# Kernel optimization log

Measured on AMD Instinct MI355X. Metric: run time of the kernel, lower is better.

Reference implementation:

```python
import jax, jax.numpy as jnp
import numpy as np

WS = 7        # window_size
SHIFT = 3     # shift_size
NH = 12       # num_heads
DIM = 384
HID = 1536    # int(dim * 4.0)
EPS = 1e-5


def _rel_index(ws):
    # relative_position_index exactly as in the torch __init__ (static, numpy)
    c = np.stack(np.meshgrid(np.arange(ws), np.arange(ws), indexing='ij')).reshape(2, -1)
    r = c[:, :, None] - c[:, None, :]            # (2, N, N)
    return jnp.asarray((r[0] + ws - 1) * (2 * ws - 1) + (r[1] + ws - 1))  # (N, N) int


def _swin_attn_mask(H, W, ws, sh):
    # standard Swin shifted-window mask: 0 within region, -100 across regions
    img = np.zeros((H, W))
    cnt = 0
    for hs in (slice(0, H - ws), slice(H - ws, H - sh), slice(H - sh, H)):
        for wsl in (slice(0, W - ws), slice(W - ws, W - sh), slice(W - sh, W)):
            img[hs, wsl] = cnt
            cnt += 1
    mw = img.reshape(H // ws, ws, W // ws, ws).transpose(0, 2, 1, 3).reshape(-1, ws * ws)
    am = mw[:, None, :] - mw[:, :, None]
    return jnp.asarray(np.where(am != 0, -100.0, 0.0).astype(np.float32))  # (nW, N, N)


def _ln(x, g, b):
    m = x.mean(-1, keepdims=True)
    v = ((x - m) ** 2).mean(-1, keepdims=True)
    return (x - m) / jnp.sqrt(v + EPS) * g + b


def setup_inputs() -> dict:
    key = jax.random.key(0)
    ks = jax.random.split(key, 12)
    B, H, W, C = 32, 56, 56, DIM
    x = jax.random.normal(ks[0], (B, H * W, C), dtype=jnp.float32)
    return {
        'x': x,
        'attn_mask': _swin_attn_mask(H, W, WS, SHIFT),
        'norm1_g': jnp.ones((C,), jnp.float32),
        'norm1_b': jnp.zeros((C,), jnp.float32),
        'qkv_w': jax.random.normal(ks[1], (C, 3 * C), jnp.float32) * 0.02,
        'qkv_b': jnp.zeros((3 * C,), jnp.float32),
        'rpb_table': jax.random.normal(ks[2], ((2 * WS - 1) ** 2, NH), jnp.float32) * 0.02,
        'proj_w': jax.random.normal(ks[3], (C, C), jnp.float32) * 0.02,
        'proj_b': jnp.zeros((C,), jnp.float32),
        'norm2_g': jnp.ones((C,), jnp.float32),
        'norm2_b': jnp.zeros((C,), jnp.float32),
        'fc1_w': jax.random.normal(ks[4], (C, HID), jnp.float32) * 0.02,
        'fc1_b': jnp.zeros((HID,), jnp.float32),
        'fc2_w': jax.random.normal(ks[5], (HID, C), jnp.float32) * 0.02,
        'fc2_b': jnp.zeros((C,), jnp.float32),
        'H': 56,
        'W': 56,
    }


def reference(x, attn_mask, norm1_g, norm1_b, qkv_w, qkv_b, rpb_table,
              proj_w, proj_b, norm2_g, norm2_b, fc1_w, fc1_b, fc2_w, fc2_b, H, W):
    B, L, C = x.shape
    hd = C // NH
    scale = hd ** -0.5
    N = WS * WS

    residual = x
    h = _ln(x, norm1_g, norm1_b).reshape(B, H, W, C)
    h = jnp.roll(h, (-SHIFT, -SHIFT), axis=(1, 2))
    # window partition -> (B*nW, N, C)
    win = h.reshape(B, H // WS, WS, W // WS, WS, C).transpose(0, 1, 3, 2, 4, 5)
    win = win.reshape(-1, N, C)
    Bn = win.shape[0]

    qkv = (win @ qkv_w + qkv_b).reshape(Bn, N, 3, NH, hd)
    q, k, v = jnp.moveaxis(qkv, 2, 0)            # each (Bn, N, NH, hd)
    q = q.transpose(0, 2, 1, 3) * scale          # (Bn, NH, N, hd)
    k = k.transpose(0, 2, 1, 3)
    v = v.transpose(0, 2, 1, 3)

    attn = jnp.einsum('bhnd,bhmd->bhnm', q, k)   # (Bn, NH, N, N)
    bias = rpb_table[_rel_index(WS)]             # (N, N, NH)
    attn = attn + bias.transpose(2, 0, 1)[None]

    nW = attn_mask.shape[0]
    attn = attn.reshape(Bn // nW, nW, NH, N, N) + attn_mask[None, :, None]
    attn = jax.nn.softmax(attn.reshape(Bn, NH, N, N), axis=-1)

    out = jnp.einsum('bhnm,bhmd->bhnd', attn, v).transpose(0, 2, 1, 3).reshape(Bn, N, C)
    out = out @ proj_w + proj_b

    # window reverse -> (B, H, W, C)
    out = out.reshape(B, H // WS, W // WS, WS, WS, C).transpose(0, 1, 3, 2, 4, 5)
    out = out.reshape(B, H, W, C)
    out = jnp.roll(out, (SHIFT, SHIFT), axis=(1, 2)).reshape(B, H * W, C)

    x = residual + out
    h2 = _ln(x, norm2_g, norm2_b)
    mlp = jax.nn.gelu(h2 @ fc1_w + fc1_b, approximate=False) @ fc2_w + fc2_b
    return x + mlp
```

## Files before the change

### kernel.cpp

```cpp
#include <hip/hip_runtime.h>
#include <stdint.h>
#include <math.h>

typedef unsigned short u16;
typedef unsigned int u32;
using short8 = __attribute__((ext_vector_type(8))) short;
using f32x4  = __attribute__((ext_vector_type(4))) float;

#define NHEADS 12
#define NTOK 49
#define CDIM 384
#define HIDDIM 1536
#define HDIM 32
#define BNWIN 2048
#define MROWS 100352
#define QKV_STRIDE ((size_t)BNWIN * NHEADS * NTOK * HDIM)
#define ATT_SCALE 0.17677669529663687f
#define AW 4

__device__ __forceinline__ float bf2f(u16 u) {
    union { unsigned int i; float f; } z; z.i = ((unsigned int)u) << 16; return z.f;
}
__device__ __forceinline__ u16 f2bf(float f) {
    union { float f; unsigned int i; } z; z.f = f;
    unsigned int i = z.i;
    i += 0x7FFFu + ((i >> 16) & 1u);
    return (u16)(i >> 16);
}
__device__ __forceinline__ float lo16(u32 u) {
    union { u32 i; float f; } z; z.i = u << 16; return z.f;
}
__device__ __forceinline__ float hi16(u32 u) {
    union { u32 i; float f; } z; z.i = u & 0xffff0000u; return z.f;
}

__device__ __forceinline__ void async16(const void* g, void* l) {
    __builtin_amdgcn_global_load_lds(
        (const __attribute__((address_space(1))) void*)g,
        (__attribute__((address_space(3))) void*)l, 16, 0, 0);
}

__global__ __launch_bounds__(256) void k_conv(const float* __restrict__ B,
    u16* __restrict__ BT, int K, int N)
{
    const int idx = blockIdx.x * 256 + threadIdx.x;
    if (idx >= K * N) return;
    const int n = idx / K, k = idx - n * K;
    BT[idx] = f2bf(B[(size_t)k * N + n]);
}

__global__ __launch_bounds__(256) void k_btab(const float* __restrict__ rpb,
    float* __restrict__ bt)
{
    const int idx = blockIdx.x * 256 + threadIdx.x;
    const int r    = idx & 3;
    const int lane = (idx >> 2) & 63;
    const int tile = (idx >> 8) & 15;
    const int h    = (idx >> 12) % NHEADS;
    const int cls  = idx / (NHEADS << 12);
    const int mt = tile >> 2, nt = tile & 3;
    const int kt = mt * 16 + (lane >> 4) * 4 + r;
    const int qt = nt * 16 + (lane & 15);
    float val;
    if (kt >= NTOK) val = -1e30f;
    else if (qt >= NTOK) val = 0.f;
    else {
        const int pk = kt / 7, qk = kt % 7, pq = qt / 7, qq = qt % 7;
        val = rpb[((pq - pk + 6) * 13 + (qq - qk + 6)) * NHEADS + h];
        const int ae = cls >> 1, be = cls & 1;
        const int regq = (ae ? ((pq < 4) ? 1 : 2) : 0) * 3 + (be ? ((qq < 4) ? 1 : 2) : 0);
        const int regk = (ae ? ((pk < 4) ? 1 : 2) : 0) * 3 + (be ? ((qk < 4) ? 1 : 2) : 0);
        if (regq != regk) val -= 100.f;
    }
    bt[idx] = val;
}

__global__ __launch_bounds__(256) void k_ln1(const float* __restrict__ x,
    const float* __restrict__ g, const float* __restrict__ b, u16* __restrict__ outw)
{
    const int lane = threadIdx.x & 63;
    const int t = blockIdx.x * 4 + (threadIdx.x >> 6);
    const int wi = t / NTOK, n = t % NTOK;
    const int bb = wi >> 6, w64 = wi & 63;
    const int p = (w64 >> 3) * 7 + n / 7;
    const int q = (w64 & 7) * 7 + n % 7;
    const int sh = (p + 3) % 56, sw = (q + 3) % 56;
    const float* row = x + ((size_t)bb * 3136 + sh * 56 + sw) * CDIM;
    float v[6]; float s = 0.f, sq = 0.f;
#pragma unroll
    for (int i = 0; i < 6; i++) {
        v[i] = row[lane + 64 * i];
        s += v[i]; sq += v[i] * v[i];
    }
#pragma unroll
    for (int off = 32; off >= 1; off >>= 1) {
        s  += __shfl_xor(s, off, 64);
        sq += __shfl_xor(sq, off, 64);
    }
    const float mean = s * (1.f / CDIM);
    const float var  = sq * (1.f / CDIM) - mean * mean;
    const float rstd = rsqrtf(var + 1e-5f);
    u16* orow = outw + (size_t)t * CDIM;
#pragma unroll
    for (int i = 0; i < 6; i++) {
        const int c = lane + 64 * i;
        orow[c] = f2bf((v[i] - mean) * rstd * g[c] + b[c]);
    }
}

__global__ __launch_bounds__(256) void k_ln2(const float* __restrict__ y,
    const float* __restrict__ g, const float* __restrict__ b, u16* __restrict__ outw)
{
    const int lane = threadIdx.x & 63;
    const int t = blockIdx.x * 4 + (threadIdx.x >> 6);
    const float* row = y + (size_t)t * CDIM;
    float v[6]; float s = 0.f, sq = 0.f;
#pragma unroll
    for (int i = 0; i < 6; i++) {
        v[i] = row[lane + 64 * i];
        s += v[i]; sq += v[i] * v[i];
    }
#pragma unroll
    for (int off = 32; off >= 1; off >>= 1) {
        s  += __shfl_xor(s, off, 64);
        sq += __shfl_xor(sq, off, 64);
    }
    const float mean = s * (1.f / CDIM);
    const float var  = sq * (1.f / CDIM) - mean * mean;
    const float rstd = rsqrtf(var + 1e-5f);
    u16* orow = outw + (size_t)t * CDIM;
#pragma unroll
    for (int i = 0; i < 6; i++) {
        const int c = lane + 64 * i;
        orow[c] = f2bf((v[i] - mean) * rstd * g[c] + b[c]);
    }
}

template<int MODE>
__global__ __launch_bounds__(256) void k_mgemm(
    const u16* __restrict__ A, const u16* __restrict__ BT,
    const float* __restrict__ bias,
    u16* __restrict__ out_bf,
    const float* res_f,
    float* out_f,
    int M, int Nn, int K)
{
    __shared__ __align__(16) u16 Als[128 * 32];
    __shared__ __align__(16) u16 Bls[128 * 32];
    const int tid = threadIdx.x;
    const int w = tid >> 6, l = tid & 63;
    const int wr = w >> 1, wc = w & 1;
    const int lrow = l & 15, quad = l >> 4;
    const int m0 = blockIdx.x * 128, n0 = blockIdx.y * 128;

    const int seg0 = tid, seg1 = tid + 256;
    const int r0 = seg0 >> 2, q0 = (seg0 & 3) ^ ((r0 >> 1) & 3);
    const int r1 = seg1 >> 2, q1 = (seg1 & 3) ^ ((r1 >> 1) & 3);
    const u16* Ag0 = A  + (size_t)(m0 + r0) * K + q0 * 8;
    const u16* Ag1 = A  + (size_t)(m0 + r1) * K + q1 * 8;
    const u16* Bg0 = BT + (size_t)(n0 + r0) * K + q0 * 8;
    const u16* Bg1 = BT + (size_t)(n0 + r1) * K + q1 * 8;
    u16* Al0 = &Als[seg0 * 8]; u16* Al1 = &Als[seg1 * 8];
    u16* Bl0 = &Bls[seg0 * 8]; u16* Bl1 = &Bls[seg1 * 8];

    const short8* afp[4]; const short8* bfp[4];
#pragma unroll
    for (int i = 0; i < 4; i++) {
        const int ra = wr * 64 + i * 16 + lrow;
        afp[i] = (const short8*)&Als[ra * 32 + ((quad ^ ((ra >> 1) & 3)) << 3)];
        const int rb = wc * 64 + i * 16 + lrow;
        bfp[i] = (const short8*)&Bls[rb * 32 + ((quad ^ ((rb >> 1) & 3)) << 3)];
    }

    f32x4 acc[4][4];
#pragma unroll
    for (int i = 0; i < 4; i++)
#pragma unroll
        for (int j = 0; j < 4; j++)
            acc[i][j] = (f32x4){0.f, 0.f, 0.f, 0.f};

    for (int k0 = 0; k0 < K; k0 += 32) {
        async16(Ag0 + k0, Al0);
        async16(Ag1 + k0, Al1);
        async16(Bg0 + k0, Bl0);
        async16(Bg1 + k0, Bl1);
        __syncthreads();
        short8 af[4], bf[4];
#pragma unroll
        for (int i = 0; i < 4; i++) { af[i] = *afp[i]; bf[i] = *bfp[i]; }
#pragma unroll
        for (int mi = 0; mi < 4; mi++)
#pragma unroll
            for (int ni = 0; ni < 4; ni++)
                acc[mi][ni] = __builtin_amdgcn_mfma_f32_16x16x32_bf16(
                    af[mi], bf[ni], acc[mi][ni], 0, 0, 0);
        __syncthreads();
    }

    const int mbase = m0 + wr * 64 + quad * 4;
    const int nbase = n0 + wc * 64 + lrow;
#pragma unroll
    for (int mi = 0; mi < 4; mi++) {
#pragma unroll
        for (int r = 0; r < 4; r++) {
            const int grow = mbase + mi * 16 + r;
            if constexpr (MODE == 0) {
                const int wi = grow / NTOK, n = grow % NTOK;
#pragma unroll
                for (int ni = 0; ni < 4; ni++) {
                    const int gcol = nbase + ni * 16;
                    float val = acc[mi][ni][r] + bias[gcol];
                    const int part = gcol / CDIM;
                    const int rem = gcol % CDIM;
                    const int hcol = rem >> 5, d = rem & 31;
                    if (part == 0) val *= ATT_SCALE;
                    out_bf[(size_t)part * QKV_STRIDE +
                           (((size_t)wi * NHEADS + hcol) * NTOK + n) * HDIM + d] = f2bf(val);
                }
            } else if constexpr (MODE == 1) {
                const int wi = grow / NTOK, n = grow % NTOK;
                const int bb = wi >> 6, w64 = wi & 63;
                const int p = (w64 >> 3) * 7 + n / 7;
                const int q = (w64 & 7) * 7 + n % 7;
                const int sh = (p + 3) % 56, sw = (q + 3) % 56;
                const size_t drow = ((size_t)bb * 3136 + sh * 56 + sw) * CDIM;
#pragma unroll
                for (int ni = 0; ni < 4; ni++) {
                    const int gcol = nbase + ni * 16;
                    out_f[drow + gcol] = res_f[drow + gcol] + acc[mi][ni][r] + bias[gcol];
                }
            } else if constexpr (MODE == 2) {
#pragma unroll
                for (int ni = 0; ni < 4; ni++) {
                    const int gcol = nbase + ni * 16;
                    const float v = acc[mi][ni][r] + bias[gcol];
                    const float gel = 0.5f * v * (1.0f + erff(v * 0.70710678118654752f));
                    out_bf[(size_t)grow * Nn + gcol] = f2bf(gel);
                }
            } else {
#pragma unroll
                for (int ni = 0; ni < 4; ni++) {
                    const int gcol = nbase + ni * 16;
                    const size_t o = (size_t)grow * Nn + gcol;
                    out_f[o] = acc[mi][ni][r] + bias[gcol] + res_f[o];
                }
            }
        }
    }
}

__global__ __launch_bounds__(64 * AW) void k_attn2(
    const u16* __restrict__ qkv, const float* __restrict__ btab,
    u16* __restrict__ ctx)
{
    __shared__ __align__(16) u16 Vt[AW][2048];
    __shared__ __align__(16) u16 Pl[AW][4096];

    const int wv = threadIdx.x >> 6, lane = threadIdx.x & 63;
    const int quad = lane >> 4, c16 = lane & 15;
    const int gwh = blockIdx.x * AW + wv;
    const int wi = gwh / NHEADS, h = gwh - wi * NHEADS;
    const u16* qb = qkv + (size_t)gwh * (NTOK * HDIM);
    const u16* kb = qb + QKV_STRIDE;
    const u16* vb = qb + 2 * QKV_STRIDE;

    u16* vt = &Vt[wv][0];
    for (int i = lane; i < 256; i += 64) {
        const int tok = i >> 2, d0 = (i & 3) * 8;
        uint4 t = make_uint4(0u, 0u, 0u, 0u);
        if (tok < NTOK) t = *(const uint4*)(vb + tok * HDIM + d0);
        const u32 w_[4] = { t.x, t.y, t.z, t.w };
#pragma unroll
        for (int j = 0; j < 8; j++) {
            const int d = d0 + j;
            const u16 val = (u16)((j & 1) ? (w_[j >> 1] >> 16) : (w_[j >> 1] & 0xffffu));
            vt[(d * 64 + tok) ^ ((d & 7) << 3) ^ (((d >> 3) & 3) << 4)] = val;
        }
    }

    short8 qf[4], kf[4];
#pragma unroll
    for (int t = 0; t < 4; t++) {
        qf[t] = *(const short8*)(qb + (t * 16 + c16) * HDIM + quad * 8);
        kf[t] = *(const short8*)(kb + (t * 16 + c16) * HDIM + quad * 8);
    }

    const int a = (wi & 63) >> 3, b = wi & 7;
    const int cls = ((a == 7) ? 2 : 0) | ((b == 7) ? 1 : 0);
    const f32x4* tb = (const f32x4*)(btab + ((size_t)(cls * NHEADS + h) << 12));

    f32x4 acc[4][4];
#pragma unroll
    for (int mt = 0; mt < 4; mt++)
#pragma unroll
        for (int nt = 0; nt < 4; nt++)
            acc[mt][nt] = __builtin_amdgcn_mfma_f32_16x16x32_bf16(
                kf[mt], qf[nt], tb[(mt * 4 + nt) * 64 + lane], 0, 0, 0);

    float inv[4];
#pragma unroll
    for (int nt = 0; nt < 4; nt++) {
        float m = -1e30f;
#pragma unroll
        for (int mt = 0; mt < 4; mt++)
#pragma unroll
            for (int r = 0; r < 4; r++) m = fmaxf(m, acc[mt][nt][r]);
        m = fmaxf(m, __shfl_xor(m, 16, 64));
        m = fmaxf(m, __shfl_xor(m, 32, 64));
        float s = 0.f;
#pragma unroll
        for (int mt = 0; mt < 4; mt++)
#pragma unroll
            for (int r = 0; r < 4; r++) {
                const float e = __expf(acc[mt][nt][r] - m);
                acc[mt][nt][r] = e;
                s += e;
            }
        s += __shfl_xor(s, 16, 64);
        s += __shfl_xor(s, 32, 64);
        inv[nt] = 1.f / s;
    }

    u16* pl = &Pl[wv][0];
#pragma unroll
    for (int nt = 0; nt < 4; nt++) {
        const int q = nt * 16 + c16;
        const int sw = (q & 7) << 3;
#pragma unroll
        for (int mt = 0; mt < 4; mt++) {
            const u32 p01 = (u32)f2bf(acc[mt][nt][0]) | ((u32)f2bf(acc[mt][nt][1]) << 16);
            const u32 p23 = (u32)f2bf(acc[mt][nt][2]) | ((u32)f2bf(acc[mt][nt][3]) << 16);
            *(uint2*)&pl[(q * 64 + mt * 16 + quad * 4) ^ sw] = make_uint2(p01, p23);
        }
    }
    __syncthreads();

    f32x4 o[2][4];
#pragma unroll
    for (int mt = 0; mt < 2; mt++)
#pragma unroll
        for (int nt = 0; nt < 4; nt++) o[mt][nt] = (f32x4){0.f, 0.f, 0.f, 0.f};
#pragma unroll
    for (int ks = 0; ks < 2; ks++) {
        short8 va[2], pb[4];
#pragma unroll
        for (int mt = 0; mt < 2; mt++) {
            const int d = mt * 16 + c16;
            va[mt] = *(const short8*)&vt[(d * 64 + ks * 32 + quad * 8)
                        ^ ((d & 7) << 3) ^ (((d >> 3) & 3) << 4)];
        }
#pragma unroll
        for (int nt = 0; nt < 4; nt++) {
            const int q = nt * 16 + c16;
            pb[nt] = *(const short8*)&pl[(q * 64 + ks * 32 + quad * 8) ^ ((q & 7) << 3)];
        }
#pragma unroll
        for (int mt = 0; mt < 2; mt++)
#pragma unroll
            for (int nt = 0; nt < 4; nt++)
                o[mt][nt] = __builtin_amdgcn_mfma_f32_16x16x32_bf16(
                    va[mt], pb[nt], o[mt][nt], 0, 0, 0);
    }

#pragma unroll
    for (int nt = 0; nt < 4; nt++) {
        const int q = nt * 16 + c16;
        if (q < NTOK) {
            u16* crow = ctx + ((size_t)wi * NTOK + q) * CDIM + h * HDIM;
#pragma unroll
            for (int mt = 0; mt < 2; mt++) {
                const u32 p01 = (u32)f2bf(o[mt][nt][0] * inv[nt])
                              | ((u32)f2bf(o[mt][nt][1] * inv[nt]) << 16);
                const u32 p23 = (u32)f2bf(o[mt][nt][2] * inv[nt])
                              | ((u32)f2bf(o[mt][nt][3] * inv[nt]) << 16);
                *(uint2*)(crow + mt * 16 + quad * 4) = make_uint2(p01, p23);
            }
        }
    }
}

extern "C" void kernel_launch(void* const* d_in, const int* in_sizes, int n_in,
                              void* d_out, int out_size, void* d_ws, size_t ws_size,
                              hipStream_t stream)
{
    (void)in_sizes; (void)n_in; (void)out_size; (void)ws_size;
    const float* x     = (const float*)d_in[0];
    const float* n1g   = (const float*)d_in[2];
    const float* n1b   = (const float*)d_in[3];
    const float* qkvw  = (const float*)d_in[4];
    const float* qkvb  = (const float*)d_in[5];
    const float* rpb   = (const float*)d_in[6];
    const float* projw = (const float*)d_in[7];
    const float* projb = (const float*)d_in[8];
    const float* n2g   = (const float*)d_in[9];
    const float* n2b   = (const float*)d_in[10];
    const float* fc1w  = (const float*)d_in[11];
    const float* fc1b  = (const float*)d_in[12];
    const float* fc2w  = (const float*)d_in[13];
    const float* fc2b  = (const float*)d_in[14];
    float* out = (float*)d_out;

    char* ws = (char*)d_ws;
    const size_t szA   = (size_t)MROWS * CDIM * 2;
    const size_t szQKV = 3 * szA;
    u16*   Abuf = (u16*)ws;
    u16*   QKV  = (u16*)(ws + szA);
    u16*   Ctx  = (u16*)(ws + szA + szQKV);
    u16*   qkvT = (u16*)(ws + szA + szQKV + szA);
    u16*   projT = qkvT + 1152 * 384;
    u16*   fc1T  = projT + 384 * 384;
    u16*   fc2T  = fc1T + 1536 * 384;
    float* btab  = (float*)(fc2T + 1536 * 384);
    u16*   H2   = Abuf;
    u16*   Mid  = QKV;

    k_conv<<<(384 * 1152 + 255) / 256, 256, 0, stream>>>(qkvw, qkvT, 384, 1152);
    k_conv<<<(384 * 384 + 255) / 256, 256, 0, stream>>>(projw, projT, 384, 384);
    k_conv<<<(384 * 1536 + 255) / 256, 256, 0, stream>>>(fc1w, fc1T, 384, 1536);
    k_conv<<<(1536 * 384 + 255) / 256, 256, 0, stream>>>(fc2w, fc2T, 1536, 384);
    k_btab<<<(4 * NHEADS * 4096) / 256, 256, 0, stream>>>(rpb, btab);

    k_ln1<<<MROWS / 4, 256, 0, stream>>>(x, n1g, n1b, Abuf);
    {
        dim3 g(MROWS / 128, 1152 / 128);
        k_mgemm<0><<<g, 256, 0, stream>>>(Abuf, qkvT, qkvb, QKV, nullptr, nullptr, MROWS, 1152, 384);
    }
    k_attn2<<<(BNWIN * NHEADS) / AW, 64 * AW, 0, stream>>>(QKV, btab, Ctx);
    {
        dim3 g(MROWS / 128, 384 / 128);
        k_mgemm<1><<<g, 256, 0, stream>>>(Ctx, projT, projb, nullptr, x, out, MROWS, 384, 384);
    }
    k_ln2<<<MROWS / 4, 256, 0, stream>>>(out, n2g, n2b, H2);
    {
        dim3 g(MROWS / 128, 1536 / 128);
        k_mgemm<2><<<g, 256, 0, stream>>>(H2, fc1T, fc1b, Mid, nullptr, nullptr, MROWS, 1536, 384);
    }
    {
        dim3 g(MROWS / 128, 384 / 128);
        k_mgemm<3><<<g, 256, 0, stream>>>(Mid, fc2T, fc2b, nullptr, out, out, MROWS, 384, 1536);
    }
}
```

Before: 1.432 ms.

## Triple-buffer GEMM LDS tiles and remap blocks across XCDs

The bf16 MFMA GEMM moves from a single LDS buffer with two barriers per K step to a three-stage ring. Global-to-LDS async copies for step t+2 are issued before computing step t, with one vmcnt wait and barrier per step, so load latency overlaps the MFMAs. The launch also becomes a 1D grid whose block IDs are remapped so each XCD (assuming 8) gets a contiguous run of tiles, improving L2 reuse of A rows across N-blocks. The cost is triple the LDS footprint, which may lower occupancy, and hand-written waitcnt logic that depends on the exact count of outstanding loads.

Measured after the change: 1.322 ms. -7.7%, faster.

```diff
diff --git a/kernel.cpp b/kernel.cpp
--- a/kernel.cpp
+++ b/kernel.cpp
@@ -143,15 +143,21 @@
     u16* __restrict__ out_bf,
     const float* res_f,
     float* out_f,
-    int M, int Nn, int K)
-{
-    __shared__ __align__(16) u16 Als[128 * 32];
-    __shared__ __align__(16) u16 Bls[128 * 32];
+    int M, int Nn, int K, int NB)
+{
+    __shared__ __align__(16) u16 Als[3][128 * 32];
+    __shared__ __align__(16) u16 Bls[3][128 * 32];
     const int tid = threadIdx.x;
     const int w = tid >> 6, l = tid & 63;
     const int wr = w >> 1, wc = w & 1;
     const int lrow = l & 15, quad = l >> 4;
-    const int m0 = blockIdx.x * 128, n0 = blockIdx.y * 128;
+
+    const int nwg = gridDim.x;
+    const int qd = nwg >> 3, rr = nwg & 7;
+    const int xcd = blockIdx.x & 7, rk = blockIdx.x >> 3;
+    const int swz = ((xcd < rr) ? xcd * (qd + 1) : rr * (qd + 1) + (xcd - rr) * qd) + rk;
+    const int mb = swz / NB, nb = swz - mb * NB;
+    const int m0 = mb * 128, n0 = nb * 128;
 
     const int seg0 = tid, seg1 = tid + 256;
     const int r0 = seg0 >> 2, q0 = (seg0 & 3) ^ ((r0 >> 1) & 3);
@@ -160,16 +166,14 @@
     const u16* Ag1 = A  + (size_t)(m0 + r1) * K + q1 * 8;
     const u16* Bg0 = BT + (size_t)(n0 + r0) * K + q0 * 8;
     const u16* Bg1 = BT + (size_t)(n0 + r1) * K + q1 * 8;
-    u16* Al0 = &Als[seg0 * 8]; u16* Al1 = &Als[seg1 * 8];
-    u16* Bl0 = &Bls[seg0 * 8]; u16* Bl1 = &Bls[seg1 * 8];
-
-    const short8* afp[4]; const short8* bfp[4];
+
+    int aoff[4], boff[4];
 #pragma unroll
     for (int i = 0; i < 4; i++) {
         const int ra = wr * 64 + i * 16 + lrow;
-        afp[i] = (const short8*)&Als[ra * 32 + ((quad ^ ((ra >> 1) & 3)) << 3)];
+        aoff[i] = ra * 32 + ((quad ^ ((ra >> 1) & 3)) << 3);
         const int rb = wc * 64 + i * 16 + lrow;
-        bfp[i] = (const short8*)&Bls[rb * 32 + ((quad ^ ((rb >> 1) & 3)) << 3)];
+        boff[i] = rb * 32 + ((quad ^ ((rb >> 1) & 3)) << 3);
     }
 
     f32x4 acc[4][4];
@@ -179,23 +183,51 @@
         for (int j = 0; j < 4; j++)
             acc[i][j] = (f32x4){0.f, 0.f, 0.f, 0.f};
 
-    for (int k0 = 0; k0 < K; k0 += 32) {
-        async16(Ag0 + k0, Al0);
-        async16(Ag1 + k0, Al1);
-        async16(Bg0 + k0, Bl0);
-        async16(Bg1 + k0, Bl1);
-        __syncthreads();
+    auto stage = [&](int buf, int k0) {
+        u16* Ald = &Als[buf][0];
+        u16* Bld = &Bls[buf][0];
+        async16(Ag0 + k0, Ald + seg0 * 8);
+        async16(Ag1 + k0, Ald + seg1 * 8);
+        async16(Bg0 + k0, Bld + seg0 * 8);
+        async16(Bg1 + k0, Bld + seg1 * 8);
+    };
+    auto compute = [&](int buf) {
+        const u16* Ab = &Als[buf][0];
+        const u16* Bb = &Bls[buf][0];
         short8 af[4], bf[4];
 #pragma unroll
-        for (int i = 0; i < 4; i++) { af[i] = *afp[i]; bf[i] = *bfp[i]; }
+        for (int i = 0; i < 4; i++) {
+            af[i] = *(const short8*)(Ab + aoff[i]);
+            bf[i] = *(const short8*)(Bb + boff[i]);
+        }
 #pragma unroll
         for (int mi = 0; mi < 4; mi++)
 #pragma unroll
             for (int ni = 0; ni < 4; ni++)
                 acc[mi][ni] = __builtin_amdgcn_mfma_f32_16x16x32_bf16(
                     af[mi], bf[ni], acc[mi][ni], 0, 0, 0);
-        __syncthreads();
-    }
+    };
+
+    const int nk = K >> 5;
+    stage(0, 0);
+    stage(1, 32);
+    asm volatile("s_waitcnt vmcnt(4)" ::: "memory");
+    __builtin_amdgcn_s_barrier();
+    __builtin_amdgcn_sched_barrier(0);
+    int cur = 0;
+    for (int t = 0; t < nk - 2; ++t) {
+        stage((t + 2) % 3, (t + 2) << 5);
+        compute(cur);
+        asm volatile("s_waitcnt vmcnt(4)" ::: "memory");
+        __builtin_amdgcn_s_barrier();
+        __builtin_amdgcn_sched_barrier(0);
+        cur = (cur + 1) % 3;
+    }
+    compute(cur);
+    asm volatile("s_waitcnt vmcnt(0)" ::: "memory");
+    __builtin_amdgcn_s_barrier();
+    __builtin_amdgcn_sched_barrier(0);
+    compute((cur + 1) % 3);
 
     const int mbase = m0 + wr * 64 + quad * 4;
     const int nbase = n0 + wc * 64 + lrow;
@@ -422,21 +454,21 @@
 
     k_ln1<<<MROWS / 4, 256, 0, stream>>>(x, n1g, n1b, Abuf);
     {
-        dim3 g(MROWS / 128, 1152 / 128);
-        k_mgemm<0><<<g, 256, 0, stream>>>(Abuf, qkvT, qkvb, QKV, nullptr, nullptr, MROWS, 1152, 384);
+        const int nb = 1152 / 128;
+        k_mgemm<0><<<(MROWS / 128) * nb, 256, 0, stream>>>(Abuf, qkvT, qkvb, QKV, nullptr, nullptr, MROWS, 1152, 384, nb);
     }
     k_attn2<<<(BNWIN * NHEADS) / AW, 64 * AW, 0, stream>>>(QKV, btab, Ctx);
     {
-        dim3 g(MROWS / 128, 384 / 128);
-        k_mgemm<1><<<g, 256, 0, stream>>>(Ctx, projT, projb, nullptr, x, out, MROWS, 384, 384);
+        const int nb = 384 / 128;
+        k_mgemm<1><<<(MROWS / 128) * nb, 256, 0, stream>>>(Ctx, projT, projb, nullptr, x, out, MROWS, 384, 384, nb);
     }
     k_ln2<<<MROWS / 4, 256, 0, stream>>>(out, n2g, n2b, H2);
     {
-        dim3 g(MROWS / 128, 1536 / 128);
-        k_mgemm<2><<<g, 256, 0, stream>>>(H2, fc1T, fc1b, Mid, nullptr, nullptr, MROWS, 1536, 384);
+        const int nb = 1536 / 128;
+        k_mgemm<2><<<(MROWS / 128) * nb, 256, 0, stream>>>(H2, fc1T, fc1b, Mid, nullptr, nullptr, MROWS, 1536, 384, nb);
     }
     {
-        dim3 g(MROWS / 128, 384 / 128);
-        k_mgemm<3><<<g, 256, 0, stream>>>(Mid, fc2T, fc2b, nullptr, out, out, MROWS, 384, 1536);
-    }
-}
+        const int nb = 384 / 128;
+        k_mgemm<3><<<(MROWS / 128) * nb, 256, 0, stream>>>(Mid, fc2T, fc2b, nullptr, out, out, MROWS, 384, 1536, nb);
+    }
+}
```
